# Kernel tuning notes

Hardware: AMD Instinct MI355X
Metric: run time of the kernel (lower is better)

## Reference

```python
import jax, jax.numpy as jnp
import numpy as np

B, C, L = 32, 256, 8192
SIGMA_SQUARED, ELL = 1.0, 50.0


def _ou_banded_chol(sigma_squared, ell, n):
    """Banded Cholesky of the tridiagonal OU precision, replicating
    scipy.linalg.cholesky_banded on the matrix built in OUProcess.__init__.
    Returns (diag, sup) of the UPPER bidiagonal factor U, where
    U[i,i] = diag[i] and U[i,i+1] = sup[i+1] (sup[0] == 0), matching
    banded_upper_prec[1] and banded_upper_prec[0] respectively."""
    corner = 1.0 / sigma_squared * (1.0 / (1.0 - np.exp(-2.0 / ell)))
    mid = 1.0 / sigma_squared * ((1.0 + np.exp(-2.0 / ell)) / (1.0 - np.exp(-2.0 / ell)))
    off = 1.0 / sigma_squared * np.exp(-1.0 / ell) / (np.exp(-2.0 / ell) - 1.0)
    a = np.full(n, mid, dtype=np.float64)
    a[0] = corner
    a[-1] = corner
    b = np.full(n - 1, off, dtype=np.float64)
    d = np.zeros(n, dtype=np.float64)
    s = np.zeros(n - 1, dtype=np.float64)
    d[0] = np.sqrt(a[0])
    for i in range(1, n):
        s[i - 1] = b[i - 1] / d[i - 1]
        d[i] = np.sqrt(a[i] - s[i - 1] ** 2)
    sup = np.concatenate([[0.0], s])
    return np.float32(d), np.float32(sup)


def setup_inputs() -> dict:
    key = jax.random.key(0)
    normal_samples = jax.random.normal(key, (B, C, L), dtype=jnp.float32)
    d, sup = _ou_banded_chol(SIGMA_SQUARED, ELL, L)
    return {
        "normal_samples": normal_samples,
        "diag": jnp.asarray(d),
        "sup": jnp.asarray(sup),
    }


def reference(normal_samples, diag, sup):
    """OUProcess.sample_gpu_dense: solve U x = z along the last axis, where U is
    upper bidiagonal (diag = U[i,i], sup[i+1] = U[i,i+1]). Backward substitution:
      x[L-1] = z[L-1] / diag[L-1]
      x[i]   = (z[i] - sup[i+1] * x[i+1]) / diag[i]
    Vectorized over (B, C) with a reverse lax.scan over L -- O(L) instead of the
    O(L^2) dense triangular solve in the torch code, same math."""
    z = jnp.moveaxis(normal_samples, 2, 0)  # (L, B, C)
    # e[i] = U[i, i+1]; e[L-1] = 0 so the first (last-index) step is z/d.
    e = jnp.concatenate([sup[1:], jnp.zeros((1,), sup.dtype)])

    def step(x_next, inp):
        z_i, d_i, e_i = inp
        x_i = (z_i - e_i * x_next) / d_i
        return x_i, x_i

    init = jnp.zeros(z.shape[1:], z.dtype)  # (B, C)
    _, xs = jax.lax.scan(step, init, (z, diag, e), reverse=True)
    return jnp.moveaxis(xs, 0, 2)  # (B, C, L)
```

## Files before the change

kernel.cpp:

```cpp
#include <hip/hip_runtime.h>


#define LN  8192
#define TPB 256
#define K   32
#define PADF(i) ((i) + ((i) >> 5))
#define LDSF (LN + (LN >> 5))

__global__ void ou_prep(const float* __restrict__ diag,
                        const float* __restrict__ sup,
                        float* __restrict__ a,
                        float* __restrict__ binv) {
    int i = blockIdx.x * blockDim.x + threadIdx.x;
    if (i < LN) {
        float inv = 1.0f / diag[i];
        binv[i] = inv;
        float e = (i + 1 < LN) ? sup[i + 1] : 0.0f;
        a[i] = -e * inv;
    }
}

__global__ __launch_bounds__(TPB) void ou_solve(
    const float* __restrict__ z,
    const float* __restrict__ a,
    const float* __restrict__ binv,
    float* __restrict__ out) {
    __shared__ float lds[LDSF];
    __shared__ float sA[TPB];
    __shared__ float sB[TPB];
    const int t = threadIdx.x;
    const long long rowbase = (long long)blockIdx.x * LN;

    {
        const float4* z4 = reinterpret_cast<const float4*>(z + rowbase);
#pragma unroll
        for (int m = 0; m < 8; ++m) {
            int gi = m * 1024 + 4 * t;
            float4 v = z4[m * 256 + t];
            int li = PADF(gi);
            lds[li + 0] = v.x; lds[li + 1] = v.y;
            lds[li + 2] = v.z; lds[li + 3] = v.w;
        }
    }

    float av[K], bv[K];
    {
        const int cb = t * K;
        const float4* a4 = reinterpret_cast<const float4*>(a + cb);
        const float4* i4 = reinterpret_cast<const float4*>(binv + cb);
        float iv[K];
#pragma unroll
        for (int j = 0; j < K / 4; ++j) {
            float4 aa = a4[j];
            float4 ii = i4[j];
            av[4 * j + 0] = aa.x; av[4 * j + 1] = aa.y;
            av[4 * j + 2] = aa.z; av[4 * j + 3] = aa.w;
            iv[4 * j + 0] = ii.x; iv[4 * j + 1] = ii.y;
            iv[4 * j + 2] = ii.z; iv[4 * j + 3] = ii.w;
        }
        __syncthreads();
        const int lb = 33 * t;
#pragma unroll
        for (int j = 0; j < K; ++j)
            bv[j] = lds[lb + j] * iv[j];
    }

    float x = 0.0f, p = 1.0f;
#pragma unroll
    for (int j = K - 1; j >= 0; --j) {
        x = fmaf(av[j], x, bv[j]);
        p *= av[j];
    }
    sA[t] = p;
    sB[t] = x;
    __syncthreads();

    for (int off = 1; off < TPB; off <<= 1) {
        float A = sA[t], Bv = sB[t];
        float A2 = 1.0f, B2 = 0.0f;
        if (t + off < TPB) { A2 = sA[t + off]; B2 = sB[t + off]; }
        float nA = A * A2;
        float nB = fmaf(A, B2, Bv);
        __syncthreads();
        sA[t] = nA;
        sB[t] = nB;
        __syncthreads();
    }
    float xcur = (t + 1 < TPB) ? sB[t + 1] : 0.0f;

    {
        const int lb = 33 * t;
#pragma unroll
        for (int j = K - 1; j >= 0; --j) {
            xcur = fmaf(av[j], xcur, bv[j]);
            lds[lb + j] = xcur;
        }
    }
    __syncthreads();

    {
        float4* o4 = reinterpret_cast<float4*>(out + rowbase);
#pragma unroll
        for (int m = 0; m < 8; ++m) {
            int gi = m * 1024 + 4 * t;
            int li = PADF(gi);
            float4 v = make_float4(lds[li + 0], lds[li + 1],
                                   lds[li + 2], lds[li + 3]);
            o4[m * 256 + t] = v;
        }
    }
}

extern "C" void kernel_launch(void* const* d_in, const int* in_sizes, int n_in,
                              void* d_out, int out_size, void* d_ws, size_t ws_size,
                              hipStream_t stream) {
    const float* z    = (const float*)d_in[0];
    const float* diag = (const float*)d_in[1];
    const float* sup  = (const float*)d_in[2];
    float* out = (float*)d_out;

    float* a    = (float*)d_ws;
    float* binv = a + LN;

    const int rows = in_sizes[0] / LN;

    ou_prep<<<(LN + TPB - 1) / TPB, TPB, 0, stream>>>(diag, sup, a, binv);
    ou_solve<<<rows, TPB, 0, stream>>>(z, a, binv, out);
}
```

Before: 455.5 us.

## Use wavefront-shuffle scan and 512 threads with 16 elements each

Doubles threads per block to 512 and halves the per-thread chunk to 16 elements. The block-wide LDS Hillis-Steele scan, which needed two barriers per step, is replaced by an in-wavefront shuffle scan plus a short serial combine of per-wave aggregates through shared memory. This removes most block barriers and shortens the serial per-thread recurrence. In exchange it adds shuffle traffic, and the larger blocks may change occupancy. The LDS padding index is adjusted to match the new chunk size.

```diff
diff --git a/kernel.cpp b/kernel.cpp
--- a/kernel.cpp
+++ b/kernel.cpp
@@ -2,8 +2,9 @@
 
 
 #define LN  8192
-#define TPB 256
-#define K   32
+#define TPB 512
+#define K   16
+#define W   (TPB / 64)
 #define PADF(i) ((i) + ((i) >> 5))
 #define LDSF (LN + (LN >> 5))
 
@@ -26,17 +27,19 @@
     const float* __restrict__ binv,
     float* __restrict__ out) {
     __shared__ float lds[LDSF];
-    __shared__ float sA[TPB];
-    __shared__ float sB[TPB];
+    __shared__ float sAw[W];
+    __shared__ float sBw[W];
     const int t = threadIdx.x;
+    const int lane = t & 63;
+    const int w = t >> 6;
     const long long rowbase = (long long)blockIdx.x * LN;
 
     {
         const float4* z4 = reinterpret_cast<const float4*>(z + rowbase);
 #pragma unroll
-        for (int m = 0; m < 8; ++m) {
-            int gi = m * 1024 + 4 * t;
-            float4 v = z4[m * 256 + t];
+        for (int m = 0; m < K / 4; ++m) {
+            int gi = m * (TPB * 4) + 4 * t;
+            float4 v = z4[m * TPB + t];
             int li = PADF(gi);
             lds[li + 0] = v.x; lds[li + 1] = v.y;
             lds[li + 2] = v.z; lds[li + 3] = v.w;
@@ -44,69 +47,75 @@
     }
 
     float av[K], bv[K];
+    const int cb = t * K;
     {
-        const int cb = t * K;
         const float4* a4 = reinterpret_cast<const float4*>(a + cb);
-        const float4* i4 = reinterpret_cast<const float4*>(binv + cb);
-        float iv[K];
 #pragma unroll
         for (int j = 0; j < K / 4; ++j) {
             float4 aa = a4[j];
-            float4 ii = i4[j];
             av[4 * j + 0] = aa.x; av[4 * j + 1] = aa.y;
             av[4 * j + 2] = aa.z; av[4 * j + 3] = aa.w;
-            iv[4 * j + 0] = ii.x; iv[4 * j + 1] = ii.y;
-            iv[4 * j + 2] = ii.z; iv[4 * j + 3] = ii.w;
         }
-        __syncthreads();
-        const int lb = 33 * t;
+    }
+    __syncthreads();
+    const int lb = 16 * t + (t >> 1);
+    {
+        const float4* i4 = reinterpret_cast<const float4*>(binv + cb);
 #pragma unroll
-        for (int j = 0; j < K; ++j)
-            bv[j] = lds[lb + j] * iv[j];
+        for (int j = 0; j < K / 4; ++j) {
+            float4 ii = i4[j];
+            bv[4 * j + 0] = lds[lb + 4 * j + 0] * ii.x;
+            bv[4 * j + 1] = lds[lb + 4 * j + 1] * ii.y;
+            bv[4 * j + 2] = lds[lb + 4 * j + 2] * ii.z;
+            bv[4 * j + 3] = lds[lb + 4 * j + 3] * ii.w;
+        }
     }
 
-    float x = 0.0f, p = 1.0f;
+    float Bx = 0.0f, Ax = 1.0f;
 #pragma unroll
     for (int j = K - 1; j >= 0; --j) {
-        x = fmaf(av[j], x, bv[j]);
-        p *= av[j];
+        Bx = fmaf(av[j], Bx, bv[j]);
+        Ax *= av[j];
     }
-    sA[t] = p;
-    sB[t] = x;
+
+#pragma unroll
+    for (int off = 1; off < 64; off <<= 1) {
+        float A2 = __shfl_down(Ax, off);
+        float B2 = __shfl_down(Bx, off);
+        if (lane + off < 64) {
+            Bx = fmaf(Ax, B2, Bx);
+            Ax *= A2;
+        }
+    }
+    if (lane == 0) { sAw[w] = Ax; sBw[w] = Bx; }
     __syncthreads();
 
-    for (int off = 1; off < TPB; off <<= 1) {
-        float A = sA[t], Bv = sB[t];
-        float A2 = 1.0f, B2 = 0.0f;
-        if (t + off < TPB) { A2 = sA[t + off]; B2 = sB[t + off]; }
-        float nA = A * A2;
-        float nB = fmaf(A, B2, Bv);
-        __syncthreads();
-        sA[t] = nA;
-        sB[t] = nB;
-        __syncthreads();
+    float Ae = 1.0f, Be = 0.0f;
+    for (int ww = w + 1; ww < W; ++ww) {
+        Be = fmaf(Ae, sBw[ww], Be);
+        Ae *= sAw[ww];
     }
-    float xcur = (t + 1 < TPB) ? sB[t + 1] : 0.0f;
 
-    {
-        const int lb = 33 * t;
+    float As = __shfl_down(Ax, 1);
+    float Bs = __shfl_down(Bx, 1);
+    if (lane == 63) { As = 1.0f; Bs = 0.0f; }
+    float xcur = fmaf(As, Be, Bs);
+
 #pragma unroll
-        for (int j = K - 1; j >= 0; --j) {
-            xcur = fmaf(av[j], xcur, bv[j]);
-            lds[lb + j] = xcur;
-        }
+    for (int j = K - 1; j >= 0; --j) {
+        xcur = fmaf(av[j], xcur, bv[j]);
+        lds[lb + j] = xcur;
     }
     __syncthreads();
 
     {
         float4* o4 = reinterpret_cast<float4*>(out + rowbase);
 #pragma unroll
-        for (int m = 0; m < 8; ++m) {
-            int gi = m * 1024 + 4 * t;
+        for (int m = 0; m < K / 4; ++m) {
+            int gi = m * (TPB * 4) + 4 * t;
             int li = PADF(gi);
-            float4 v = make_float4(lds[li + 0], lds[li + 1],
-                                   lds[li + 2], lds[li + 3]);
-            o4[m * 256 + t] = v;
+            o4[m * TPB + t] = make_float4(lds[li + 0], lds[li + 1],
+                                          lds[li + 2], lds[li + 3]);
         }
     }
 }
```

After: 431.0 us. 1.06x faster.
